# Performance work log

Hardware: AMD Instinct MI355X
Metric: run time of the kernel (lower is better)

## Reference

```python
import jax, jax.numpy as jnp
import numpy as np

D_MODEL = 1024
N_HEADS = 16
HEAD_DIM = D_MODEL // N_HEADS
D_FF = 4 * D_MODEL
LN_EPS = 1e-5  # torch nn.LayerNorm default


def setup_inputs() -> dict:
    key = jax.random.key(0)
    ks = jax.random.split(key, 6)
    B, T = 2, 2048
    s = lambda fan_in: 1.0 / np.sqrt(fan_in)
    return {
        "x": jax.random.normal(ks[0], (B, T, D_MODEL), dtype=jnp.float32),
        # weights stored as [in, out]
        "w_qkv": jax.random.normal(ks[1], (D_MODEL, 3 * D_MODEL), dtype=jnp.float32) * s(D_MODEL),
        "w_proj": jax.random.normal(ks[2], (D_MODEL, D_MODEL), dtype=jnp.float32) * s(D_MODEL),
        "ln1_g": jnp.ones((D_MODEL,), jnp.float32),
        "ln1_b": jnp.zeros((D_MODEL,), jnp.float32),
        "ln2_g": jnp.ones((D_MODEL,), jnp.float32),
        "ln2_b": jnp.zeros((D_MODEL,), jnp.float32),
        "w_ff1": jax.random.normal(ks[3], (D_MODEL, D_FF), dtype=jnp.float32) * s(D_MODEL),
        "b_ff1": jnp.zeros((D_FF,), jnp.float32),
        "w_ff2": jax.random.normal(ks[4], (D_FF, D_MODEL), dtype=jnp.float32) * s(D_FF),
        "b_ff2": jnp.zeros((D_MODEL,), jnp.float32),
    }


def _layernorm(x, g, b):
    mu = jnp.mean(x, axis=-1, keepdims=True)
    var = jnp.mean(jnp.square(x - mu), axis=-1, keepdims=True)
    return (x - mu) * jax.lax.rsqrt(var + LN_EPS) * g + b


def _attention(x, w_qkv, w_proj):
    B, T, C = x.shape
    qkv = x @ w_qkv  # [B,T,3C]
    q, k, v = jnp.split(qkv, 3, axis=-1)
    # [B, H, T, Dh]
    q = q.reshape(B, T, N_HEADS, HEAD_DIM).transpose(0, 2, 1, 3)
    k = k.reshape(B, T, N_HEADS, HEAD_DIM).transpose(0, 2, 1, 3)
    v = v.reshape(B, T, N_HEADS, HEAD_DIM).transpose(0, 2, 1, 3)
    att = jnp.einsum("bhqd,bhkd->bhqk", q, k) / np.sqrt(HEAD_DIM).astype(np.float32)
    causal = jnp.tril(jnp.ones((T, T), dtype=bool))
    att = jnp.where(causal, att, -jnp.inf)
    att = jax.nn.softmax(att, axis=-1)
    y = jnp.einsum("bhqk,bhkd->bhqd", att, v)
    y = y.transpose(0, 2, 1, 3).reshape(B, T, C)
    return y @ w_proj


def _ffn(x, w1, b1, w2, b2):
    h = jax.nn.gelu(x @ w1 + b1, approximate=False)  # torch nn.GELU default is exact
    return h @ w2 + b2


def reference(x, w_qkv, w_proj, ln1_g, ln1_b, ln2_g, ln2_b, w_ff1, b_ff1, w_ff2, b_ff2):
    x = x + _attention(_layernorm(x, ln1_g, ln1_b), w_qkv, w_proj)
    x = x + _ffn(_layernorm(x, ln2_g, ln2_b), w_ff1, b_ff1, w_ff2, b_ff2)
    return x
```

## Files before the change

kernel.cpp:

```cpp
#include <hip/hip_runtime.h>
#include <hip/hip_bf16.h>

typedef unsigned short u16;
typedef unsigned int u32;
typedef unsigned long long u64;
typedef __bf16 bf16x8 __attribute__((ext_vector_type(8)));
typedef float f32x4 __attribute__((ext_vector_type(4)));
typedef u16 u16x8 __attribute__((ext_vector_type(8)));

#define LN_EPS 1e-5f
#define SCALE_L2E 0.18033688011112042f

__device__ inline float bf2f(u16 u) { return __uint_as_float(((u32)u) << 16); }
__device__ inline u16 f2b(float f) {
    u32 u = __float_as_uint(f);
    u32 r = (u + 0x7fffu + ((u >> 16) & 1u)) >> 16;
    return (u16)r;
}
__device__ inline u32 cvtpk(float a, float b) {
    u32 r;
    asm("v_cvt_pk_bf16_f32 %0, %1, %2" : "=v"(r) : "v"(a), "v"(b));
    return r;
}

typedef __attribute__((address_space(3))) u32 as3_u32;
typedef const __attribute__((address_space(1))) u32 as1_u32;
__device__ inline void gl_lds16(const u16* g, u16* l) {
    __builtin_amdgcn_global_load_lds((as1_u32*)g, (as3_u32*)l, 16, 0, 0);
}

__global__ __launch_bounds__(256) void cast_transpose_k(const float* __restrict__ W,
                                                        u16* __restrict__ WT, int K, int N) {
    __shared__ float tile[64][65];
    int n0 = blockIdx.x * 64, k0 = blockIdx.y * 64;
    int t = threadIdx.x;
#pragma unroll
    for (int i = 0; i < 4; i++) {
        int idx = t + i * 256;
        int r = idx >> 4;
        int cq = idx & 15;
        float4 v = *reinterpret_cast<const float4*>(&W[(size_t)(k0 + r) * N + n0 + cq * 4]);
        tile[r][cq * 4 + 0] = v.x; tile[r][cq * 4 + 1] = v.y;
        tile[r][cq * 4 + 2] = v.z; tile[r][cq * 4 + 3] = v.w;
    }
    __syncthreads();
#pragma unroll
    for (int i = 0; i < 2; i++) {
        int c = t + i * 256;
        int n = c >> 3;
        int k8 = (c & 7) * 8;
        u16x8 o;
#pragma unroll
        for (int j = 0; j < 8; j++) o[j] = f2b(tile[k8 + j][n]);
        *reinterpret_cast<u16x8*>(&WT[(size_t)(n0 + n) * K + k0 + k8]) = o;
    }
}

__global__ __launch_bounds__(256) void layernorm_k(const float* __restrict__ X,
                                                   const float* __restrict__ g,
                                                   const float* __restrict__ b,
                                                   u16* __restrict__ out) {
    int row = blockIdx.x;
    int t = threadIdx.x;
    float4 v = *reinterpret_cast<const float4*>(&X[(size_t)row * 1024 + t * 4]);
    float s = v.x + v.y + v.z + v.w;
    float s2 = v.x * v.x + v.y * v.y + v.z * v.z + v.w * v.w;
#pragma unroll
    for (int o = 1; o < 64; o <<= 1) {
        s += __shfl_xor(s, o, 64);
        s2 += __shfl_xor(s2, o, 64);
    }
    __shared__ float ws[4], ws2[4];
    int wid = t >> 6, lane = t & 63;
    if (lane == 0) { ws[wid] = s; ws2[wid] = s2; }
    __syncthreads();
    float ts = ws[0] + ws[1] + ws[2] + ws[3];
    float ts2 = ws2[0] + ws2[1] + ws2[2] + ws2[3];
    float mu = ts * (1.0f / 1024.0f);
    float var = ts2 * (1.0f / 1024.0f) - mu * mu;
    float rs = rsqrtf(var + LN_EPS);
    float4 gg = *reinterpret_cast<const float4*>(&g[t * 4]);
    float4 bb = *reinterpret_cast<const float4*>(&b[t * 4]);
    u16 o4[4];
    o4[0] = f2b((v.x - mu) * rs * gg.x + bb.x);
    o4[1] = f2b((v.y - mu) * rs * gg.y + bb.y);
    o4[2] = f2b((v.z - mu) * rs * gg.z + bb.z);
    o4[3] = f2b((v.w - mu) * rs * gg.w + bb.w);
    *reinterpret_cast<ulonglong1*>(&out[(size_t)row * 1024 + t * 4]) =
        *reinterpret_cast<ulonglong1*>(o4);
}

__global__ __launch_bounds__(512, 2) void gemm256_k(const u16* __restrict__ A,
                                                    const u16* __restrict__ Bt,
                                                    int M, int N, int K,
                                                    const float* __restrict__ bias,
                                                    int do_gelu,
                                                    u16* __restrict__ outB) {
    __shared__ u16 As[2][256 * 64];
    __shared__ u16 Bs[2][256 * 64];
    int gx = gridDim.x;
    int nwg = gx * gridDim.y;
    int id = blockIdx.y * gx + blockIdx.x;
    int id2 = (nwg & 7) ? id : ((id & 7) * (nwg >> 3) + (id >> 3));
    int bx = id2 % gx, by = id2 / gx;
    int m0 = by * 256, n0 = bx * 256;
    int t = threadIdx.x;
    int w = t >> 6, lane = t & 63;
    int lr = lane & 15, lg = lane >> 4;
    int wm = (w >> 2) * 128, wn = (w & 3) * 64;
    f32x4 acc[8][4] = {};

    auto stage = [&](int buf, int kt) {
        int k0 = kt * 64;
#pragma unroll
        for (int i = 0; i < 4; i++) {
            int c = t + i * 512;
            int row = c >> 3, pch = c & 7;
            gl_lds16(&A[(size_t)(m0 + row) * K + k0 + ((pch ^ (row & 7)) * 8)],
                     &As[buf][c * 8]);
        }
#pragma unroll
        for (int i = 0; i < 4; i++) {
            int c = t + i * 512;
            int row = c >> 3, pch = c & 7;
            gl_lds16(&Bt[(size_t)(n0 + row) * K + k0 + ((pch ^ (row & 7)) * 8)],
                     &Bs[buf][c * 8]);
        }
    };

    int nk = K >> 6;
    stage(0, 0);
    __syncthreads();
    for (int kt = 0; kt < nk; kt++) {
        int cur = kt & 1;
        if (kt + 1 < nk) stage(cur ^ 1, kt + 1);
#pragma unroll
        for (int ks = 0; ks < 2; ks++) {
            bf16x8 af[8], bfr[4];
#pragma unroll
            for (int mi = 0; mi < 8; mi++) {
                int row = wm + mi * 16 + lr;
                af[mi] = *reinterpret_cast<const bf16x8*>(
                    &As[cur][row * 64 + (((ks * 4 + lg) ^ (row & 7)) * 8)]);
            }
#pragma unroll
            for (int ni = 0; ni < 4; ni++) {
                int row = wn + ni * 16 + lr;
                bfr[ni] = *reinterpret_cast<const bf16x8*>(
                    &Bs[cur][row * 64 + (((ks * 4 + lg) ^ (row & 7)) * 8)]);
            }
            __builtin_amdgcn_s_setprio(1);
#pragma unroll
            for (int mi = 0; mi < 8; mi++)
#pragma unroll
                for (int ni = 0; ni < 4; ni++)
                    acc[mi][ni] = __builtin_amdgcn_mfma_f32_16x16x32_bf16(
                        af[mi], bfr[ni], acc[mi][ni], 0, 0, 0);
            __builtin_amdgcn_s_setprio(0);
        }
        __syncthreads();
    }

#pragma unroll
    for (int mi = 0; mi < 8; mi++) {
#pragma unroll
        for (int ni = 0; ni < 4; ni++) {
            int col = n0 + wn + ni * 16 + lr;
#pragma unroll
            for (int i = 0; i < 4; i++) {
                int row = m0 + wm + mi * 16 + lg * 4 + i;
                float v = acc[mi][ni][i];
                if (bias) v += bias[col];
                if (do_gelu) v = 0.5f * v * (1.0f + erff(v * 0.70710678118f));
                outB[(size_t)row * N + col] = f2b(v);
            }
        }
    }
}

__global__ __launch_bounds__(256) void gemm_k(const u16* __restrict__ A,
                                              const u16* __restrict__ Bt,
                                              int M, int N, int K,
                                              const float* __restrict__ bias,
                                              const float* __restrict__ resid,
                                              int do_gelu,
                                              float* __restrict__ outF,
                                              u16* __restrict__ outB) {
    __shared__ u16 As[2][128 * 64];
    __shared__ u16 Bs[2][64 * 64];
    int gx = gridDim.x;
    int nwg = gx * gridDim.y;
    int id = blockIdx.y * gx + blockIdx.x;
    int id2 = (nwg & 7) ? id : ((id & 7) * (nwg >> 3) + (id >> 3));
    int bx = id2 % gx, by = id2 / gx;
    int m0 = by * 128, n0 = bx * 64;
    int t = threadIdx.x;
    int w = t >> 6, lane = t & 63;
    int lr = lane & 15, lg = lane >> 4;
    int wm = (w >> 1) * 64, wn = (w & 1) * 32;
    f32x4 acc[4][2] = {};

    auto stage = [&](int buf, int kt) {
        int k0 = kt * 64;
#pragma unroll
        for (int i = 0; i < 4; i++) {
            int c = t + i * 256;
            int row = c >> 3, pch = c & 7;
            gl_lds16(&A[(size_t)(m0 + row) * K + k0 + ((pch ^ (row & 7)) * 8)],
                     &As[buf][c * 8]);
        }
#pragma unroll
        for (int i = 0; i < 2; i++) {
            int c = t + i * 256;
            int row = c >> 3, pch = c & 7;
            gl_lds16(&Bt[(size_t)(n0 + row) * K + k0 + ((pch ^ (row & 7)) * 8)],
                     &Bs[buf][c * 8]);
        }
    };

    int nk = K >> 6;
    stage(0, 0);
    __syncthreads();
    for (int kt = 0; kt < nk; kt++) {
        int cur = kt & 1;
        if (kt + 1 < nk) stage(cur ^ 1, kt + 1);
#pragma unroll
        for (int ks = 0; ks < 2; ks++) {
            bf16x8 af[4], bfr[2];
#pragma unroll
            for (int mi = 0; mi < 4; mi++) {
                int row = wm + mi * 16 + lr;
                af[mi] = *reinterpret_cast<const bf16x8*>(
                    &As[cur][row * 64 + (((ks * 4 + lg) ^ (row & 7)) * 8)]);
            }
#pragma unroll
            for (int ni = 0; ni < 2; ni++) {
                int row = wn + ni * 16 + lr;
                bfr[ni] = *reinterpret_cast<const bf16x8*>(
                    &Bs[cur][row * 64 + (((ks * 4 + lg) ^ (row & 7)) * 8)]);
            }
            __builtin_amdgcn_s_setprio(1);
#pragma unroll
            for (int mi = 0; mi < 4; mi++)
#pragma unroll
                for (int ni = 0; ni < 2; ni++)
                    acc[mi][ni] = __builtin_amdgcn_mfma_f32_16x16x32_bf16(
                        af[mi], bfr[ni], acc[mi][ni], 0, 0, 0);
            __builtin_amdgcn_s_setprio(0);
        }
        __syncthreads();
    }
#pragma unroll
    for (int mi = 0; mi < 4; mi++) {
#pragma unroll
        for (int ni = 0; ni < 2; ni++) {
            int col = n0 + wn + ni * 16 + lr;
#pragma unroll
            for (int i = 0; i < 4; i++) {
                int row = m0 + wm + mi * 16 + lg * 4 + i;
                float v = acc[mi][ni][i];
                if (bias) v += bias[col];
                if (do_gelu) v = 0.5f * v * (1.0f + erff(v * 0.70710678118f));
                if (resid) v += resid[(size_t)row * N + col];
                if (outF) outF[(size_t)row * N + col] = v;
                else outB[(size_t)row * N + col] = f2b(v);
            }
        }
    }
}

__global__ __launch_bounds__(256) void attn_k(const u16* __restrict__ QKV, u16* __restrict__ Y) {
    __shared__ u16 Ks[64 * 64];
    __shared__ u16 Vt[64 * 64];
    __shared__ u16 Pt[4][16 * 64];
    int u = (blockIdx.x + blockIdx.y) & 31;
    int vv = (u & 8) ? (u ^ 7) : u;
    int qt = 31 - vv;
    int bh = blockIdx.y;
    int b = bh >> 4, h = bh & 15;
    int t = threadIdx.x;
    int w = t >> 6, lane = t & 63;
    int lr = lane & 15, lg = lane >> 4;
    int q_g = qt * 64 + w * 16 + lr;
    size_t bhbase = (size_t)b * 2048 * 3072 + h * 64;

    bf16x8 qf[2];
#pragma unroll
    for (int ks = 0; ks < 2; ks++)
        qf[ks] = *reinterpret_cast<const bf16x8*>(&QKV[bhbase + (size_t)q_g * 3072 + ks * 32 + lg * 8]);

    float l = 0.0f;
    f32x4 oacc[4] = {};

    int vkey = t & 63;
    int vd0 = (t >> 6) * 8;
    int nkv = qt + 1;

    for (int kt = 0; kt < nkv; kt++) {
        size_t tb = bhbase + (size_t)(kt * 64) * 3072;
#pragma unroll
        for (int i = 0; i < 2; i++) {
            int c = t + i * 256;
            int key = c >> 3, pch = c & 7;
            gl_lds16(&QKV[tb + (size_t)key * 3072 + 1024 + ((pch ^ (key & 7)) * 8)], &Ks[c * 8]);
        }
        u16x8 vreg[2];
#pragma unroll
        for (int i = 0; i < 2; i++)
            vreg[i] = *reinterpret_cast<const u16x8*>(&QKV[tb + (size_t)vkey * 3072 + 2048 + vd0 + i * 32]);
#pragma unroll
        for (int i = 0; i < 2; i++)
#pragma unroll
            for (int j = 0; j < 8; j++) {
                int d = vd0 + i * 32 + j;
                Vt[(d * 64 + vkey) ^ ((d & 7) << 3)] = vreg[i][j];
            }
        __syncthreads();

        int kbmax = (kt == qt) ? (w + 1) : 4;
        f32x4 s[4];
        __builtin_amdgcn_s_setprio(1);
#pragma unroll
        for (int kb = 0; kb < 4; kb++) {
            if (kb < kbmax) {
                int key = kb * 16 + lr;
                bf16x8 k0 = *reinterpret_cast<const bf16x8*>(&Ks[key * 64 + ((lg ^ (key & 7)) * 8)]);
                bf16x8 k1 = *reinterpret_cast<const bf16x8*>(&Ks[key * 64 + (((4 + lg) ^ (key & 7)) * 8)]);
                f32x4 z = {0, 0, 0, 0};
                z = __builtin_amdgcn_mfma_f32_16x16x32_bf16(k0, qf[0], z, 0, 0, 0);
                s[kb] = __builtin_amdgcn_mfma_f32_16x16x32_bf16(k1, qf[1], z, 0, 0, 0);
            }
        }
        __builtin_amdgcn_s_setprio(0);

        float p[16];
        float ps4[4];
        bool diag = (kt == qt);
#pragma unroll
        for (int kb = 0; kb < 4; kb++) {
            ps4[kb] = 0.0f;
            if (kb < kbmax) {
#pragma unroll
                for (int i2 = 0; i2 < 4; i2++) {
                    float v = s[kb][i2] * SCALE_L2E;
                    if (diag && kb == w)
                        v = (kb * 16 + lg * 4 + i2 <= w * 16 + lr) ? v : -1e30f;
                    p[kb * 4 + i2] = exp2f(v);
                }
                ps4[kb] = (p[kb * 4 + 0] + p[kb * 4 + 1]) + (p[kb * 4 + 2] + p[kb * 4 + 3]);
            }
        }
        float ps = (ps4[0] + ps4[1]) + (ps4[2] + ps4[3]);
        ps += __shfl_xor(ps, 16, 64);
        ps += __shfl_xor(ps, 32, 64);
        l += ps;
#pragma unroll
        for (int kb = 0; kb < 4; kb++) {
            u32 d0 = 0, d1 = 0;
            if (kb < kbmax) {
                d0 = cvtpk(p[kb * 4 + 0], p[kb * 4 + 1]);
                d1 = cvtpk(p[kb * 4 + 2], p[kb * 4 + 3]);
            }
            int eidx = (lr * 64 + kb * 16 + lg * 4) ^ ((lr & 7) << 3);
            *reinterpret_cast<u64*>(&Pt[w][eidx]) = (u64)d0 | ((u64)d1 << 32);
        }
        __builtin_amdgcn_s_setprio(1);
#pragma unroll
        for (int ks = 0; ks < 2; ks++) {
            bf16x8 pb = *reinterpret_cast<const bf16x8*>(&Pt[w][(lr * 64 + ks * 32 + lg * 8) ^ ((lr & 7) << 3)]);
#pragma unroll
            for (int db = 0; db < 4; db++) {
                int d = db * 16 + lr;
                bf16x8 va = *reinterpret_cast<const bf16x8*>(&Vt[(d * 64 + ks * 32 + lg * 8) ^ ((d & 7) << 3)]);
                oacc[db] = __builtin_amdgcn_mfma_f32_16x16x32_bf16(va, pb, oacc[db], 0, 0, 0);
            }
        }
        __builtin_amdgcn_s_setprio(0);
        __syncthreads();
    }

    float inv = 1.0f / l;
#pragma unroll
    for (int db = 0; db < 4; db++) {
        u32 lo = cvtpk(oacc[db][0] * inv, oacc[db][1] * inv);
        u32 hi = cvtpk(oacc[db][2] * inv, oacc[db][3] * inv);
        size_t ya = (size_t)(b * 2048 + q_g) * 1024 + h * 64 + db * 16 + lg * 4;
        *reinterpret_cast<u32*>(&Y[ya]) = lo;
        *reinterpret_cast<u32*>(&Y[ya + 2]) = hi;
    }
}

extern "C" void kernel_launch(void* const* d_in, const int* in_sizes, int n_in,
                              void* d_out, int out_size, void* d_ws, size_t ws_size,
                              hipStream_t stream) {
    const float* x      = (const float*)d_in[0];
    const float* w_qkv  = (const float*)d_in[1];
    const float* w_proj = (const float*)d_in[2];
    const float* ln1_g  = (const float*)d_in[3];
    const float* ln1_b  = (const float*)d_in[4];
    const float* ln2_g  = (const float*)d_in[5];
    const float* ln2_b  = (const float*)d_in[6];
    const float* w_ff1  = (const float*)d_in[7];
    const float* b_ff1  = (const float*)d_in[8];
    const float* w_ff2  = (const float*)d_in[9];
    const float* b_ff2  = (const float*)d_in[10];
    float* out = (float*)d_out;

    char* ws = (char*)d_ws;
    u16* qkv    = (u16*)(ws);
    u16* act16  = (u16*)(ws + 25165824);
    float* x2   = (float*)(ws + 33554432);
    u16* hbuf   = (u16*)(ws + 50331648);
    u16* wqkvT  = (u16*)(ws + 83886080);
    u16* wprojT = (u16*)(ws + 90177536);
    u16* wff1T  = (u16*)(ws + 92274688);
    u16* wff2T  = (u16*)(ws + 100663296);

    cast_transpose_k<<<dim3(48, 16), 256, 0, stream>>>(w_qkv, wqkvT, 1024, 3072);
    cast_transpose_k<<<dim3(16, 16), 256, 0, stream>>>(w_proj, wprojT, 1024, 1024);
    cast_transpose_k<<<dim3(64, 16), 256, 0, stream>>>(w_ff1, wff1T, 1024, 4096);
    cast_transpose_k<<<dim3(16, 64), 256, 0, stream>>>(w_ff2, wff2T, 4096, 1024);

    layernorm_k<<<4096, 256, 0, stream>>>(x, ln1_g, ln1_b, act16);
    gemm256_k<<<dim3(12, 16), 512, 0, stream>>>(act16, wqkvT, 4096, 3072, 1024,
                                                nullptr, 0, qkv);
    attn_k<<<dim3(32, 32), 256, 0, stream>>>(qkv, act16);
    gemm_k<<<dim3(16, 32), 256, 0, stream>>>(act16, wprojT, 4096, 1024, 1024,
                                             nullptr, x, 0, x2, nullptr);
    layernorm_k<<<4096, 256, 0, stream>>>(x2, ln2_g, ln2_b, act16);
    gemm256_k<<<dim3(16, 16), 512, 0, stream>>>(act16, wff1T, 4096, 4096, 1024,
                                                b_ff1, 1, hbuf);
    gemm_k<<<dim3(16, 32), 256, 0, stream>>>(hbuf, wff2T, 4096, 1024, 4096,
                                             b_ff2, x2, 0, out, nullptr);
}
```

Measured before the change: 304.0 us.

## Shrink big GEMM tile to 256x64, add XCD-aware block mapping, pack V transpose

Replaces the 256x256, 512-thread GEMM used for the QKV and FF1 projections with a 256x64 tile on 256 threads. This gives many more workgroups to fill the CUs, at the cost of less B-tile reuse per block. Adds an xcd_map helper that assigns blocks to 8x-wide column groups per XCD for L2 locality, used by both GEMMs. In attention, the V transpose into LDS now loads two keys per thread and writes packed 32-bit pairs instead of scalar 16-bit stores, cutting LDS store count.

```diff
diff --git a/kernel.cpp b/kernel.cpp
--- a/kernel.cpp
+++ b/kernel.cpp
@@ -27,6 +27,21 @@
 typedef const __attribute__((address_space(1))) u32 as1_u32;
 __device__ inline void gl_lds16(const u16* g, u16* l) {
     __builtin_amdgcn_global_load_lds((as1_u32*)g, (as3_u32*)l, 16, 0, 0);
+}
+
+__device__ inline void xcd_map(int gx, int gy, int& bx, int& by) {
+    int nwg = gx * gy;
+    int id = blockIdx.y * gx + blockIdx.x;
+    int nrc = gx >> 3;
+    int cpx = nwg >> 3;
+    if (((nwg | gx) & 7) == 0 && (cpx & 7) == 0 && nrc >= 1 && (8 % nrc) == 0) {
+        int xcd = id & 7, loc = id >> 3, rh = cpx >> 3;
+        bx = (xcd % nrc) * 8 + (loc & 7);
+        by = (xcd / nrc) * rh + (loc >> 3);
+    } else {
+        int id2 = (nwg & 7) ? id : ((id & 7) * (nwg >> 3) + (id >> 3));
+        bx = id2 % gx; by = id2 / gx;
+    }
 }
 
 __global__ __launch_bounds__(256) void cast_transpose_k(const float* __restrict__ W,
@@ -90,38 +105,35 @@
         *reinterpret_cast<ulonglong1*>(o4);
 }
 
-__global__ __launch_bounds__(512, 2) void gemm256_k(const u16* __restrict__ A,
-                                                    const u16* __restrict__ Bt,
-                                                    int M, int N, int K,
-                                                    const float* __restrict__ bias,
-                                                    int do_gelu,
-                                                    u16* __restrict__ outB) {
+__global__ __launch_bounds__(256, 2) void gemmA_k(const u16* __restrict__ A,
+                                                  const u16* __restrict__ Bt,
+                                                  int M, int N, int K,
+                                                  const float* __restrict__ bias,
+                                                  int do_gelu,
+                                                  u16* __restrict__ outB) {
     __shared__ u16 As[2][256 * 64];
-    __shared__ u16 Bs[2][256 * 64];
-    int gx = gridDim.x;
-    int nwg = gx * gridDim.y;
-    int id = blockIdx.y * gx + blockIdx.x;
-    int id2 = (nwg & 7) ? id : ((id & 7) * (nwg >> 3) + (id >> 3));
-    int bx = id2 % gx, by = id2 / gx;
-    int m0 = by * 256, n0 = bx * 256;
+    __shared__ u16 Bs[2][64 * 64];
+    int bx, by;
+    xcd_map(gridDim.x, gridDim.y, bx, by);
+    int m0 = by * 256, n0 = bx * 64;
     int t = threadIdx.x;
     int w = t >> 6, lane = t & 63;
     int lr = lane & 15, lg = lane >> 4;
-    int wm = (w >> 2) * 128, wn = (w & 3) * 64;
-    f32x4 acc[8][4] = {};
+    int wm = w * 64;
+    f32x4 acc[4][4] = {};
 
     auto stage = [&](int buf, int kt) {
         int k0 = kt * 64;
 #pragma unroll
-        for (int i = 0; i < 4; i++) {
-            int c = t + i * 512;
+        for (int i = 0; i < 8; i++) {
+            int c = t + i * 256;
             int row = c >> 3, pch = c & 7;
             gl_lds16(&A[(size_t)(m0 + row) * K + k0 + ((pch ^ (row & 7)) * 8)],
                      &As[buf][c * 8]);
         }
 #pragma unroll
-        for (int i = 0; i < 4; i++) {
-            int c = t + i * 512;
+        for (int i = 0; i < 2; i++) {
+            int c = t + i * 256;
             int row = c >> 3, pch = c & 7;
             gl_lds16(&Bt[(size_t)(n0 + row) * K + k0 + ((pch ^ (row & 7)) * 8)],
                      &Bs[buf][c * 8]);
@@ -136,22 +148,22 @@
         if (kt + 1 < nk) stage(cur ^ 1, kt + 1);
 #pragma unroll
         for (int ks = 0; ks < 2; ks++) {
-            bf16x8 af[8], bfr[4];
-#pragma unroll
-            for (int mi = 0; mi < 8; mi++) {
+            bf16x8 af[4], bfr[4];
+#pragma unroll
+            for (int mi = 0; mi < 4; mi++) {
                 int row = wm + mi * 16 + lr;
                 af[mi] = *reinterpret_cast<const bf16x8*>(
                     &As[cur][row * 64 + (((ks * 4 + lg) ^ (row & 7)) * 8)]);
             }
 #pragma unroll
             for (int ni = 0; ni < 4; ni++) {
-                int row = wn + ni * 16 + lr;
+                int row = ni * 16 + lr;
                 bfr[ni] = *reinterpret_cast<const bf16x8*>(
                     &Bs[cur][row * 64 + (((ks * 4 + lg) ^ (row & 7)) * 8)]);
             }
             __builtin_amdgcn_s_setprio(1);
 #pragma unroll
-            for (int mi = 0; mi < 8; mi++)
+            for (int mi = 0; mi < 4; mi++)
 #pragma unroll
                 for (int ni = 0; ni < 4; ni++)
                     acc[mi][ni] = __builtin_amdgcn_mfma_f32_16x16x32_bf16(
@@ -162,10 +174,10 @@
     }
 
 #pragma unroll
-    for (int mi = 0; mi < 8; mi++) {
+    for (int mi = 0; mi < 4; mi++) {
 #pragma unroll
         for (int ni = 0; ni < 4; ni++) {
-            int col = n0 + wn + ni * 16 + lr;
+            int col = n0 + ni * 16 + lr;
 #pragma unroll
             for (int i = 0; i < 4; i++) {
                 int row = m0 + wm + mi * 16 + lg * 4 + i;
@@ -188,11 +200,8 @@
                                               u16* __restrict__ outB) {
     __shared__ u16 As[2][128 * 64];
     __shared__ u16 Bs[2][64 * 64];
-    int gx = gridDim.x;
-    int nwg = gx * gridDim.y;
-    int id = blockIdx.y * gx + blockIdx.x;
-    int id2 = (nwg & 7) ? id : ((id & 7) * (nwg >> 3) + (id >> 3));
-    int bx = id2 % gx, by = id2 / gx;
+    int bx, by;
+    xcd_map(gridDim.x, gridDim.y, bx, by);
     int m0 = by * 128, n0 = bx * 64;
     int t = threadIdx.x;
     int w = t >> 6, lane = t & 63;
@@ -292,8 +301,8 @@
     float l = 0.0f;
     f32x4 oacc[4] = {};
 
-    int vkey = t & 63;
-    int vd0 = (t >> 6) * 8;
+    int vkey0 = (t & 31) * 2;
+    int vd0 = (t >> 5) * 8;
     int nkv = qt + 1;
 
     for (int kt = 0; kt < nkv; kt++) {
@@ -304,17 +313,14 @@
             int key = c >> 3, pch = c & 7;
             gl_lds16(&QKV[tb + (size_t)key * 3072 + 1024 + ((pch ^ (key & 7)) * 8)], &Ks[c * 8]);
         }
-        u16x8 vreg[2];
-#pragma unroll
-        for (int i = 0; i < 2; i++)
-            vreg[i] = *reinterpret_cast<const u16x8*>(&QKV[tb + (size_t)vkey * 3072 + 2048 + vd0 + i * 32]);
-#pragma unroll
-        for (int i = 0; i < 2; i++)
-#pragma unroll
-            for (int j = 0; j < 8; j++) {
-                int d = vd0 + i * 32 + j;
-                Vt[(d * 64 + vkey) ^ ((d & 7) << 3)] = vreg[i][j];
-            }
+        u16x8 va = *reinterpret_cast<const u16x8*>(&QKV[tb + (size_t)vkey0 * 3072 + 2048 + vd0]);
+        u16x8 vb = *reinterpret_cast<const u16x8*>(&QKV[tb + (size_t)(vkey0 + 1) * 3072 + 2048 + vd0]);
+#pragma unroll
+        for (int j = 0; j < 8; j++) {
+            int d = vd0 + j;
+            int eidx = (d * 64 + vkey0) ^ ((d & 7) << 3);
+            *reinterpret_cast<u32*>(&Vt[eidx]) = (u32)va[j] | ((u32)vb[j] << 16);
+        }
         __syncthreads();
 
         int kbmax = (kt == qt) ? (w + 1) : 4;
@@ -371,8 +377,8 @@
 #pragma unroll
             for (int db = 0; db < 4; db++) {
                 int d = db * 16 + lr;
-                bf16x8 va = *reinterpret_cast<const bf16x8*>(&Vt[(d * 64 + ks * 32 + lg * 8) ^ ((d & 7) << 3)]);
-                oacc[db] = __builtin_amdgcn_mfma_f32_16x16x32_bf16(va, pb, oacc[db], 0, 0, 0);
+                bf16x8 vva = *reinterpret_cast<const bf16x8*>(&Vt[(d * 64 + ks * 32 + lg * 8) ^ ((d & 7) << 3)]);
+                oacc[db] = __builtin_amdgcn_mfma_f32_16x16x32_bf16(vva, pb, oacc[db], 0, 0, 0);
             }
         }
         __builtin_amdgcn_s_setprio(0);
@@ -422,14 +428,14 @@
     cast_transpose_k<<<dim3(16, 64), 256, 0, stream>>>(w_ff2, wff2T, 4096, 1024);
 
     layernorm_k<<<4096, 256, 0, stream>>>(x, ln1_g, ln1_b, act16);
-    gemm256_k<<<dim3(12, 16), 512, 0, stream>>>(act16, wqkvT, 4096, 3072, 1024,
-                                                nullptr, 0, qkv);
+    gemmA_k<<<dim3(48, 16), 256, 0, stream>>>(act16, wqkvT, 4096, 3072, 1024,
+                                              nullptr, 0, qkv);
     attn_k<<<dim3(32, 32), 256, 0, stream>>>(qkv, act16);
     gemm_k<<<dim3(16, 32), 256, 0, stream>>>(act16, wprojT, 4096, 1024, 1024,
                                              nullptr, x, 0, x2, nullptr);
     layernorm_k<<<4096, 256, 0, stream>>>(x2, ln2_g, ln2_b, act16);
-    gemm256_k<<<dim3(16, 16), 512, 0, stream>>>(act16, wff1T, 4096, 4096, 1024,
-                                                b_ff1, 1, hbuf);
+    gemmA_k<<<dim3(64, 16), 256, 0, stream>>>(act16, wff1T, 4096, 4096, 1024,
+                                              b_ff1, 1, hbuf);
     gemm_k<<<dim3(16, 32), 256, 0, stream>>>(hbuf, wff2T, 4096, 1024, 4096,
                                              b_ff2, x2, 0, out, nullptr);
 }
```

Measured after the change: 304.8 us. No clear change (+0.3%).
